# Kernel tuning notes

Hardware: AMD Instinct MI355X
Metric: run time of the kernel (lower is better)

## Reference

```python
import jax, jax.numpy as jnp
import numpy as np

N_HEAD = 16
D_HEAD = 64
D_MODEL = 1024
D_INNER = 4096
QLEN = 1024
MLEN = 1024
BSZ = 2
LN_EPS = 1e-5


def _layer_norm(x, g, b, eps=LN_EPS):
    mu = jnp.mean(x, axis=-1, keepdims=True)
    var = jnp.var(x, axis=-1, keepdims=True)
    return (x - mu) * jax.lax.rsqrt(var + eps) * g + b


def _rel_shift(x):
    # x: [qlen, rlen, bsz, n_head]
    q, r, b, n = x.shape
    zp = jnp.zeros((q, 1, b, n), x.dtype)
    xp = jnp.concatenate([zp, x], axis=1).reshape(r + 1, q, b, n)
    return xp[1:].reshape(q, r, b, n)


def setup_inputs() -> dict:
    key = jax.random.key(0)
    ks = jax.random.split(key, 12)
    klen = MLEN + QLEN
    w = jax.random.normal(ks[0], (QLEN, BSZ, D_MODEL), jnp.float32)
    r = jax.random.normal(ks[1], (klen, D_MODEL), jnp.float32)
    mems = jax.random.normal(ks[2], (MLEN, BSZ, D_MODEL), jnp.float32)
    # causal mask: query i attends keys j <= i + mlen
    i = jnp.arange(QLEN)[:, None]
    j = jnp.arange(klen)[None, :]
    attn_mask = (j > i + MLEN)[:, :, None]  # [qlen, klen, 1] bool
    s = 0.02
    params = dict(
        qkv_w=jax.random.normal(ks[3], (3 * N_HEAD * D_HEAD, D_MODEL), jnp.float32) * s,
        r_net_w=jax.random.normal(ks[4], (N_HEAD * D_HEAD, D_MODEL), jnp.float32) * s,
        o_w=jax.random.normal(ks[5], (D_MODEL, N_HEAD * D_HEAD), jnp.float32) * s,
        r_r_bias=jax.random.normal(ks[6], (N_HEAD, D_HEAD), jnp.float32) * s,
        r_w_bias=jax.random.normal(ks[7], (N_HEAD, D_HEAD), jnp.float32) * s,
        ln1_g=jnp.ones((D_MODEL,), jnp.float32),
        ln1_b=jnp.zeros((D_MODEL,), jnp.float32),
        ff_w1=jax.random.normal(ks[8], (D_INNER, D_MODEL), jnp.float32) * s,
        ff_b1=jnp.zeros((D_INNER,), jnp.float32),
        ff_w2=jax.random.normal(ks[9], (D_MODEL, D_INNER), jnp.float32) * s,
        ff_b2=jnp.zeros((D_MODEL,), jnp.float32),
        ln2_g=jnp.ones((D_MODEL,), jnp.float32),
        ln2_b=jnp.zeros((D_MODEL,), jnp.float32),
    )
    return dict(w=w, r=r, mems=mems, attn_mask=attn_mask, **params)


def reference(w, r, mems, attn_mask, qkv_w, r_net_w, o_w, r_r_bias, r_w_bias,
              ln1_g, ln1_b, ff_w1, ff_b1, ff_w2, ff_b2, ln2_g, ln2_b):
    qlen, bsz = w.shape[0], w.shape[1]
    scale = 1.0 / (D_HEAD ** 0.5)
    cat = jnp.concatenate([mems, w], axis=0)              # [klen, b, d_model]
    klen = cat.shape[0]
    w_heads = cat @ qkv_w.T                                # [klen, b, 3*n*d]
    wq, wk, wv = jnp.split(w_heads, 3, axis=-1)
    wq = wq[-qlen:]
    r_head_k = (r @ r_net_w.T).reshape(-1, N_HEAD, D_HEAD)  # [rlen, n, d]
    wq = wq.reshape(qlen, bsz, N_HEAD, D_HEAD)
    wk = wk.reshape(klen, bsz, N_HEAD, D_HEAD)
    wv = wv.reshape(klen, bsz, N_HEAD, D_HEAD)
    AC = jnp.einsum('ibnd,jbnd->ijbn', wq + r_w_bias, wk)   # content term
    BD = jnp.einsum('ibnd,jnd->ijbn', wq + r_r_bias, r_head_k)
    BD = _rel_shift(BD)                                     # position term
    attn_score = (AC + BD) * scale
    mask_value = jnp.finfo(attn_score.dtype).min
    attn_score = jnp.where(attn_mask[:, :, :, None], mask_value, attn_score)
    attn_prob = jax.nn.softmax(attn_score, axis=1)
    attn_vec = jnp.einsum('ijbn,jbnd->ibnd', attn_prob, wv)
    attn_vec = attn_vec.reshape(qlen, bsz, N_HEAD * D_HEAD)
    attn_out = attn_vec @ o_w.T
    h = _layer_norm(w + attn_out, ln1_g, ln1_b)             # post-lnorm
    core = jax.nn.relu(h @ ff_w1.T + ff_b1) @ ff_w2.T + ff_b2
    out = _layer_norm(h + core, ln2_g, ln2_b)
    return out
```

## Files before the change

### kernel.cpp

```cpp
#include <hip/hip_runtime.h>
#include <math.h>

#define QLEN 1024
#define MLEN 1024
#define KLEN 2048
#define BSZc 2
#define NH 16
#define DH 64
#define DM 1024
#define DI 4096

typedef unsigned short ushort_t;
typedef __attribute__((ext_vector_type(8))) short short8;
typedef __attribute__((ext_vector_type(4))) float f32x4;

__device__ __forceinline__ ushort_t f2bf(float x) {
    unsigned int u = __float_as_uint(x);
    unsigned int r = (u + 0x7FFFu + ((u >> 16) & 1u)) >> 16;
    return (ushort_t)r;
}
__device__ __forceinline__ float bf2f(ushort_t b) {
    return __uint_as_float(((unsigned int)b) << 16);
}

__device__ __forceinline__ void gload_lds16(const ushort_t* g, ushort_t* l) {
    __builtin_amdgcn_global_load_lds(
        (const __attribute__((address_space(1))) unsigned int*)g,
        (__attribute__((address_space(3))) unsigned int*)l,
        16, 0, 0);
}

__device__ __forceinline__ void cast8(const float* s, ushort_t* d, int g) {
    const float4 a = *(const float4*)(s + g * 8);
    const float4 b = *(const float4*)(s + g * 8 + 4);
    short8 o;
    o[0] = (short)f2bf(a.x); o[1] = (short)f2bf(a.y);
    o[2] = (short)f2bf(a.z); o[3] = (short)f2bf(a.w);
    o[4] = (short)f2bf(b.x); o[5] = (short)f2bf(b.y);
    o[6] = (short)f2bf(b.z); o[7] = (short)f2bf(b.w);
    *(short8*)(d + g * 8) = o;
}

__global__ __launch_bounds__(256)
void cast_phase1(const float* __restrict__ qkv_w, const float* __restrict__ rnet_w,
                 const float* __restrict__ mems, const float* __restrict__ w,
                 const float* __restrict__ r,
                 ushort_t* __restrict__ W1, ushort_t* __restrict__ W2,
                 ushort_t* __restrict__ Acat, ushort_t* __restrict__ Rsrc)
{
    int g = blockIdx.x * 256 + threadIdx.x;
    if (g < 393216)            { cast8(qkv_w,  W1,              g); }
    else if (g < 524288)       { cast8(rnet_w, W2,              g - 393216); }
    else if (g < 786432)       { cast8(mems,   Acat,            g - 524288); }
    else if (g < 1048576)      { cast8(w,      Acat + 2097152,  g - 786432); }
    else if (g < 1310720)      { cast8(r,      Rsrc,            g - 1048576); }
}

__global__ __launch_bounds__(256)
void cast_phase2(const float* __restrict__ o_w, const float* __restrict__ ffw1,
                 const float* __restrict__ ffw2,
                 ushort_t* __restrict__ W3, ushort_t* __restrict__ W4,
                 ushort_t* __restrict__ W5)
{
    int g = blockIdx.x * 256 + threadIdx.x;
    if (g < 131072)            { cast8(o_w,  W3, g); }
    else if (g < 655360)       { cast8(ffw1, W4, g - 131072); }
    else if (g < 1179648)      { cast8(ffw2, W5, g - 655360); }
}

template<int EMODE, int ACT, int BN>
__global__ __launch_bounds__(256)
void gemm_mfma(const ushort_t* __restrict__ A, const ushort_t* __restrict__ B,
               const float* __restrict__ bias,
               void* __restrict__ O0, void* __restrict__ O1,
               void* __restrict__ O2, void* __restrict__ O3,
               const float* __restrict__ rwb, const float* __restrict__ rrb,
               int M, int N, int K)
{
    constexpr int JT = BN / 32;
    __shared__ ushort_t At[128 * 32];
    __shared__ ushort_t Bt[BN * 32];

    const int tid  = threadIdx.x;
    const int lane = tid & 63;
    const int w    = tid >> 6;
    const int lr   = lane & 15;
    const int quad = lane >> 4;
    const int m0   = blockIdx.x * 128;
    const int n0   = blockIdx.y * BN;
    const int wm0  = (w >> 1) * 64;
    const int wn0  = (w & 1) * (BN / 2);

    f32x4 acc[4][JT];
#pragma unroll
    for (int it = 0; it < 4; ++it)
#pragma unroll
        for (int jt = 0; jt < JT; ++jt) acc[it][jt] = (f32x4){0.f, 0.f, 0.f, 0.f};

    const int srow = lane >> 2;
    const int scol = (lane & 3) << 3;
    const ushort_t* Ag = A + (size_t)(m0 + w * 32 + srow) * K + scol;
    ushort_t* lA0 = At + (w * 32) * 32;
    ushort_t* lA1 = At + (w * 32 + 16) * 32;
    const ushort_t* Bg;
    ushort_t *lB0, *lB1 = nullptr;
    if (BN == 128) {
        Bg  = B + (size_t)(n0 + w * 32 + srow) * K + scol;
        lB0 = Bt + (w * 32) * 32;
        lB1 = Bt + (w * 32 + 16) * 32;
    } else {
        Bg  = B + (size_t)(n0 + w * 16 + srow) * K + scol;
        lB0 = Bt + (w * 16) * 32;
    }

    const ushort_t* Ato = At + (wm0 + lr) * 32 + quad * 8;
    const ushort_t* Bto = Bt + (wn0 + lr) * 32 + quad * 8;

    for (int k0 = 0; k0 < K; k0 += 32) {
        __syncthreads();
        gload_lds16(Ag + k0, lA0);
        gload_lds16(Ag + (size_t)16 * K + k0, lA1);
        gload_lds16(Bg + k0, lB0);
        if (BN == 128) gload_lds16(Bg + (size_t)16 * K + k0, lB1);
        __syncthreads();

        short8 af[4], bf[JT];
#pragma unroll
        for (int it = 0; it < 4; ++it)
            af[it] = *(const short8*)(Ato + it * 16 * 32);
#pragma unroll
        for (int jt = 0; jt < JT; ++jt)
            bf[jt] = *(const short8*)(Bto + jt * 16 * 32);
#pragma unroll
        for (int it = 0; it < 4; ++it)
#pragma unroll
            for (int jt = 0; jt < JT; ++jt)
                acc[it][jt] = __builtin_amdgcn_mfma_f32_16x16x32_bf16(
                    af[it], bf[jt], acc[it][jt], 0, 0, 0);
    }

#pragma unroll
    for (int it = 0; it < 4; ++it)
#pragma unroll
        for (int jt = 0; jt < JT; ++jt)
#pragma unroll
            for (int rg = 0; rg < 4; ++rg) {
                const int m = m0 + wm0 + it * 16 + quad * 4 + rg;
                const int n = n0 + wn0 + jt * 16 + lr;
                float v = acc[it][jt][rg];
                if (EMODE == 0) {
                    if (bias) v += bias[n];
                    ((float*)O0)[(size_t)m * N + n] = v;
                } else if (EMODE == 1) {
                    const int j = m >> 1, b = m & 1;
                    const int part = n >> 10, hh = (n >> 6) & 15, d = n & 63;
                    if (part == 0) {
                        if (j >= MLEN) {
                            const int qi = j - MLEN;
                            const size_t qidx = (((size_t)(b * NH + hh)) * QLEN + qi) * DH + d;
                            ((ushort_t*)O0)[qidx] = f2bf(v + rwb[hh * DH + d]);
                            ((ushort_t*)O1)[qidx] = f2bf(v + rrb[hh * DH + d]);
                        }
                    } else if (part == 1) {
                        ((ushort_t*)O2)[(((size_t)(b * NH + hh)) * KLEN + j) * DH + d] = f2bf(v);
                    } else {
                        ((ushort_t*)O3)[(((size_t)(b * NH + hh)) * DH + d) * KLEN + j] = f2bf(v);
                    }
                } else if (EMODE == 2) {
                    const int hh = n >> 6, d = n & 63;
                    ((ushort_t*)O0)[(((size_t)hh) * KLEN + m) * DH + d] = f2bf(v);
                } else {
                    v += bias[n];
                    if (ACT == 1) v = fmaxf(v, 0.f);
                    ((ushort_t*)O0)[(size_t)m * N + n] = f2bf(v);
                }
            }
}

__global__ __launch_bounds__(256)
void attn_mfma(const ushort_t* __restrict__ Qac, const ushort_t* __restrict__ Qbd,
               const ushort_t* __restrict__ Kb, const ushort_t* __restrict__ Vt,
               const ushort_t* __restrict__ Rb, ushort_t* __restrict__ AV)
{
    __shared__ ushort_t Kt[64][72];
    __shared__ ushort_t Rt[128][72];
    __shared__ ushort_t Vl[64][72];
    __shared__ ushort_t Bw[4][16][84];

    const int tid  = threadIdx.x;
    const int lane = tid & 63;
    const int w    = tid >> 6;
    const int lr   = lane & 15;
    const int quad = lane >> 4;
    const int bh   = blockIdx.y;
    const int qt   = (bh & 16) ? (15 - (int)blockIdx.x) : (int)blockIdx.x;
    const int i0   = qt << 6;
    const int h    = bh & 15;
    const int b    = bh >> 4;

    short8 qaf[2], qbf[2];
    {
        const size_t rowoff = ((size_t)bh * QLEN + i0 + w * 16 + lr) * DH;
#pragma unroll
        for (int kt = 0; kt < 2; ++kt) {
            qaf[kt] = *(const short8*)(Qac + rowoff + kt * 32 + quad * 8);
            qbf[kt] = *(const short8*)(Qbd + rowoff + kt * 32 + quad * 8);
        }
    }

    f32x4 O[4];
#pragma unroll
    for (int nt = 0; nt < 4; ++nt) O[nt] = (f32x4){0.f, 0.f, 0.f, 0.f};
    float m_run = -3.4e38f, l_run = 0.f;

    const int nc  = qt + 17;
    const int stw = 3 - w;
    const float SC = 0.125f * 1.44269504f;
    const ushort_t* Kh = Kb + (size_t)bh * KLEN * DH;
    const ushort_t* Vh = Vt + (size_t)bh * DH * KLEN;
    const ushort_t* Rh = Rb + (size_t)h * KLEN * DH;

    for (int c = 0; c < nc; ++c) {
        const int j0 = c << 6;
        const int wb = 960 - i0 + j0;
        __syncthreads();
#pragma unroll
        for (int t = 0; t < 2; ++t) {
            int f = tid + (t << 8);
            int row = f >> 3, c8 = (f & 7) << 3;
            *(int4*)&Kt[row][c8] = *(const int4*)(Kh + (size_t)(j0 + row) * DH + c8);
        }
#pragma unroll
        for (int t = 0; t < 2; ++t) {
            int f = tid + (t << 8);
            int d = f >> 3, c8 = (f & 7) << 3;
            *(int4*)&Vl[d][c8] = *(const int4*)(Vh + (size_t)d * KLEN + j0 + c8);
        }
        {
            const int npass = (c == 0) ? 4 : 2;
            const int gb    = (c == 0) ? wb : wb + 64;
            for (int t = 0; t < npass; ++t) {
                int f = tid + (t << 8);
                int rl2 = f >> 3, c8 = (f & 7) << 3;
                int g = gb + rl2;
                int gc = g > (KLEN - 1) ? (KLEN - 1) : g;
                *(int4*)&Rt[g & 127][c8] = *(const int4*)(Rh + (size_t)gc * DH + c8);
            }
        }
        __syncthreads();

#pragma unroll
        for (int ctl = 0; ctl < 5; ++ctl) {
            const int wr = (stw + ctl) * 16 + lr;
            const int ring = (wb + wr) & 127;
            f32x4 z = (f32x4){0.f, 0.f, 0.f, 0.f};
#pragma unroll
            for (int kt = 0; kt < 2; ++kt) {
                short8 rb2 = *(const short8*)&Rt[ring][kt * 32 + quad * 8];
                z = __builtin_amdgcn_mfma_f32_16x16x32_bf16(qbf[kt], rb2, z, 0, 0, 0);
            }
#pragma unroll
            for (int rg = 0; rg < 4; ++rg)
                Bw[w][quad * 4 + rg][ctl * 16 + lr] = f2bf(z[rg]);
        }
#pragma unroll
        for (int ct = 0; ct < 4; ++ct) {
            f32x4 z = (f32x4){0.f, 0.f, 0.f, 0.f};
#pragma unroll
            for (int kt = 0; kt < 2; ++kt) {
                short8 kb2 = *(const short8*)&Kt[ct * 16 + lr][kt * 32 + quad * 8];
                z = __builtin_amdgcn_mfma_f32_16x16x32_bf16(qaf[kt], kb2, z, 0, 0, 0);
            }
#pragma unroll
            for (int rg = 0; rg < 4; ++rg) {
                const int rrow = quad * 4 + rg;
                ushort_t* p = &Bw[w][rrow][ct * 16 + lr + 15 - rrow];
                *p = f2bf(bf2f(*p) + z[rg]);
            }
        }

        const int lim = i0 + w * 16 + lr + 1024 - j0;
        float pv[16];
        float mx = -3.4e38f;
#pragma unroll
        for (int kt = 0; kt < 2; ++kt)
#pragma unroll
            for (int t = 0; t < 8; ++t) {
                const int jj = kt * 32 + quad * 8 + t;
                float s = bf2f(Bw[w][lr][jj + 15 - lr]) * SC;
                s = (jj > lim) ? -3.4e38f : s;
                pv[kt * 8 + t] = s;
                mx = fmaxf(mx, s);
            }
        mx = fmaxf(mx, __shfl_xor(mx, 16, 64));
        mx = fmaxf(mx, __shfl_xor(mx, 32, 64));
        const float m_new = fmaxf(m_run, mx);
        float ps = 0.f;
        short8 pf[2];
#pragma unroll
        for (int kt = 0; kt < 2; ++kt)
#pragma unroll
            for (int t = 0; t < 8; ++t) {
                const float e = exp2f(pv[kt * 8 + t] - m_new);
                ps += e;
                pf[kt][t] = (short)f2bf(e);
            }
        ps += __shfl_xor(ps, 16, 64);
        ps += __shfl_xor(ps, 32, 64);
        const float alpha = exp2f(m_run - m_new);
        m_run = m_new;
        l_run = l_run * alpha + ps;

        float ar[4];
#pragma unroll
        for (int rg = 0; rg < 4; ++rg)
            ar[rg] = __shfl(alpha, quad * 4 + rg, 64);
#pragma unroll
        for (int nt = 0; nt < 4; ++nt) {
            O[nt][0] *= ar[0]; O[nt][1] *= ar[1];
            O[nt][2] *= ar[2]; O[nt][3] *= ar[3];
        }
#pragma unroll
        for (int kt = 0; kt < 2; ++kt)
#pragma unroll
            for (int nt = 0; nt < 4; ++nt) {
                short8 vb = *(const short8*)&Vl[nt * 16 + lr][kt * 32 + quad * 8];
                O[nt] = __builtin_amdgcn_mfma_f32_16x16x32_bf16(pf[kt], vb, O[nt], 0, 0, 0);
            }
    }

    float rlv[4];
#pragma unroll
    for (int rg = 0; rg < 4; ++rg)
        rlv[rg] = 1.f / __shfl(l_run, quad * 4 + rg, 64);
#pragma unroll
    for (int nt = 0; nt < 4; ++nt)
#pragma unroll
        for (int rg = 0; rg < 4; ++rg) {
            const int i = i0 + w * 16 + quad * 4 + rg;
            AV[((size_t)i * BSZc + b) * DM + h * DH + nt * 16 + lr] = f2bf(O[nt][rg] * rlv[rg]);
        }
}

__global__ __launch_bounds__(256)
void add_ln(const float* __restrict__ X, const float* __restrict__ Y,
            const float* __restrict__ gg, const float* __restrict__ bb,
            float* __restrict__ out, ushort_t* __restrict__ outb)
{
    const int row  = blockIdx.x;
    const int tid  = threadIdx.x;
    const int lane = tid & 63;
    const int w    = tid >> 6;
    __shared__ float ssum[4], ssq[4];

    const float4 xv = ((const float4*)(X + (size_t)row * DM))[tid];
    const float4 yv = ((const float4*)(Y + (size_t)row * DM))[tid];
    const float v0 = xv.x + yv.x, v1 = xv.y + yv.y;
    const float v2 = xv.z + yv.z, v3 = xv.w + yv.w;
    float s = v0 + v1 + v2 + v3;
    float q = v0 * v0 + v1 * v1 + v2 * v2 + v3 * v3;
#pragma unroll
    for (int off = 32; off > 0; off >>= 1) {
        s += __shfl_xor(s, off, 64);
        q += __shfl_xor(q, off, 64);
    }
    if (lane == 0) { ssum[w] = s; ssq[w] = q; }
    __syncthreads();
    s = ssum[0] + ssum[1] + ssum[2] + ssum[3];
    q = ssq[0] + ssq[1] + ssq[2] + ssq[3];
    const float mean = s * (1.f / DM);
    const float var  = q * (1.f / DM) - mean * mean;
    const float rs   = rsqrtf(var + 1e-5f);
    const float4 g4 = ((const float4*)gg)[tid];
    const float4 b4 = ((const float4*)bb)[tid];
    float4 ov;
    ov.x = (v0 - mean) * rs * g4.x + b4.x;
    ov.y = (v1 - mean) * rs * g4.y + b4.y;
    ov.z = (v2 - mean) * rs * g4.z + b4.z;
    ov.w = (v3 - mean) * rs * g4.w + b4.w;
    ((float4*)(out + (size_t)row * DM))[tid] = ov;
    if (outb) {
        ushort_t* p = outb + (size_t)row * DM + tid * 4;
        p[0] = f2bf(ov.x); p[1] = f2bf(ov.y);
        p[2] = f2bf(ov.z); p[3] = f2bf(ov.w);
    }
}

extern "C" void kernel_launch(void* const* d_in, const int* in_sizes, int n_in,
                              void* d_out, int out_size, void* d_ws, size_t ws_size,
                              hipStream_t stream)
{
    (void)in_sizes; (void)n_in; (void)out_size; (void)ws_size;
    const float* w      = (const float*)d_in[0];
    const float* r      = (const float*)d_in[1];
    const float* mems   = (const float*)d_in[2];
    const float* qkv_w  = (const float*)d_in[4];
    const float* rnet_w = (const float*)d_in[5];
    const float* o_w    = (const float*)d_in[6];
    const float* r_r_b  = (const float*)d_in[7];
    const float* r_w_b  = (const float*)d_in[8];
    const float* ln1g   = (const float*)d_in[9];
    const float* ln1b   = (const float*)d_in[10];
    const float* ffw1   = (const float*)d_in[11];
    const float* ffb1   = (const float*)d_in[12];
    const float* ffw2   = (const float*)d_in[13];
    const float* ffb2   = (const float*)d_in[14];
    const float* ln2g   = (const float*)d_in[15];
    const float* ln2b   = (const float*)d_in[16];
    float* out = (float*)d_out;

    char* wsb = (char*)d_ws;
    const size_t MB = 1024 * 1024;
    ushort_t* W1    = (ushort_t*)(wsb + 0 * MB);
    ushort_t* W2    = (ushort_t*)(wsb + 6 * MB);
    ushort_t* Acat  = (ushort_t*)(wsb + 8 * MB);
    ushort_t* Rsrc  = (ushort_t*)(wsb + 16 * MB);
    ushort_t* Qac   = (ushort_t*)(wsb + 20 * MB);
    ushort_t* Qbd   = (ushort_t*)(wsb + 24 * MB);
    ushort_t* Kbf   = (ushort_t*)(wsb + 28 * MB);
    ushort_t* Vt    = (ushort_t*)(wsb + 36 * MB);
    ushort_t* Rh    = (ushort_t*)(wsb + 44 * MB);
    ushort_t* AVec  = (ushort_t*)(wsb + 0 * MB);
    ushort_t* W3    = (ushort_t*)(wsb + 4 * MB);
    float*    AOut  = (float*)(wsb + 8 * MB);
    float*    Hbuf  = (float*)(wsb + 16 * MB);
    ushort_t* Hbf   = (ushort_t*)(wsb + 24 * MB);
    ushort_t* W4    = (ushort_t*)(wsb + 28 * MB);
    ushort_t* FFbf  = (ushort_t*)(wsb + 36 * MB);
    ushort_t* W5    = (ushort_t*)(wsb + 52 * MB);
    float*    Core  = (float*)(wsb + 0 * MB);

    dim3 blk(256);

    cast_phase1<<<dim3(5120), blk, 0, stream>>>(qkv_w, rnet_w, mems, w, r,
                                                W1, W2, Acat, Rsrc);

    gemm_mfma<1, 0, 128><<<dim3(32, 24), blk, 0, stream>>>(
        Acat, W1, nullptr, Qac, Qbd, Kbf, Vt, r_w_b, r_r_b, 4096, 3072, 1024);

    gemm_mfma<2, 0, 64><<<dim3(16, 16), blk, 0, stream>>>(
        Rsrc, W2, nullptr, Rh, nullptr, nullptr, nullptr, nullptr, nullptr,
        2048, 1024, 1024);

    attn_mfma<<<dim3(QLEN / 64, BSZc * NH), blk, 0, stream>>>(
        Qac, Qbd, Kbf, Vt, Rh, AVec);

    cast_phase2<<<dim3(4608), blk, 0, stream>>>(o_w, ffw1, ffw2, W3, W4, W5);

    gemm_mfma<0, 0, 64><<<dim3(16, 16), blk, 0, stream>>>(
        AVec, W3, nullptr, AOut, nullptr, nullptr, nullptr, nullptr, nullptr,
        2048, 1024, 1024);

    add_ln<<<dim3(2 * QLEN), blk, 0, stream>>>(w, AOut, ln1g, ln1b, Hbuf, Hbf);

    gemm_mfma<3, 1, 128><<<dim3(16, 32), blk, 0, stream>>>(
        Hbf, W4, ffb1, FFbf, nullptr, nullptr, nullptr, nullptr, nullptr,
        2048, 4096, 1024);

    gemm_mfma<0, 0, 64><<<dim3(16, 16), blk, 0, stream>>>(
        FFbf, W5, ffb2, Core, nullptr, nullptr, nullptr, nullptr, nullptr,
        2048, 1024, 4096);

    add_ln<<<dim3(2 * QLEN), blk, 0, stream>>>(Hbuf, Core, ln2g, ln2b, out, nullptr);
}
```

Measured before the change: 460.0 us.

## Split attention KV range across two blocks, merge partials, fuse QKV and R GEMMs

The attention kernel now splits each query tile's key chunks between two blocks (even and odd chunks). Each block writes unnormalized fp32 partial outputs plus its running max and sum, and a new merge kernel combines them into the bf16 attention vector. This doubles the grid to raise occupancy on the many-CU GPU, at the cost of extra fp32 partial traffic and one more launch. The QKV and R projection GEMMs are fused into one launch. The position-score scratch moves from bf16 to fp32 and the R ring buffer is replaced by a full reload per chunk, which adds loads but removes the ring indexing.

```diff
diff --git a/kernel.cpp b/kernel.cpp
--- a/kernel.cpp
+++ b/kernel.cpp
@@ -18,9 +18,6 @@
     unsigned int u = __float_as_uint(x);
     unsigned int r = (u + 0x7FFFu + ((u >> 16) & 1u)) >> 16;
     return (ushort_t)r;
-}
-__device__ __forceinline__ float bf2f(ushort_t b) {
-    return __uint_as_float(((unsigned int)b) << 16);
 }
 
 __device__ __forceinline__ void gload_lds16(const ushort_t* g, ushort_t* l) {
@@ -72,10 +69,7 @@
 __global__ __launch_bounds__(256)
 void gemm_mfma(const ushort_t* __restrict__ A, const ushort_t* __restrict__ B,
                const float* __restrict__ bias,
-               void* __restrict__ O0, void* __restrict__ O1,
-               void* __restrict__ O2, void* __restrict__ O3,
-               const float* __restrict__ rwb, const float* __restrict__ rrb,
-               int M, int N, int K)
+               void* __restrict__ O0, int M, int N, int K)
 {
     constexpr int JT = BN / 32;
     __shared__ ushort_t At[128 * 32];
@@ -151,28 +145,108 @@
                 if (EMODE == 0) {
                     if (bias) v += bias[n];
                     ((float*)O0)[(size_t)m * N + n] = v;
-                } else if (EMODE == 1) {
+                } else {
+                    v += bias[n];
+                    if (ACT == 1) v = fmaxf(v, 0.f);
+                    ((ushort_t*)O0)[(size_t)m * N + n] = f2bf(v);
+                }
+            }
+}
+
+__global__ __launch_bounds__(256)
+void gemm_qkvr(const ushort_t* __restrict__ Acat, const ushort_t* __restrict__ W1,
+               const ushort_t* __restrict__ Rsrc, const ushort_t* __restrict__ W2,
+               ushort_t* __restrict__ Qac, ushort_t* __restrict__ Qbd,
+               ushort_t* __restrict__ Kbf, ushort_t* __restrict__ Vtb,
+               ushort_t* __restrict__ Rh,
+               const float* __restrict__ rwb, const float* __restrict__ rrb)
+{
+    __shared__ ushort_t At[128 * 32];
+    __shared__ ushort_t Bt[128 * 32];
+
+    const int bid  = blockIdx.x;
+    const bool isr = bid >= 768;
+    const ushort_t* A; const ushort_t* B; int m0, n0;
+    if (!isr) { A = Acat; B = W1; m0 = (bid & 31) * 128; n0 = (bid >> 5) * 128; }
+    else { int t = bid - 768; A = Rsrc; B = W2; m0 = (t & 15) * 128; n0 = (t >> 4) * 128; }
+    const int K = 1024;
+
+    const int tid  = threadIdx.x;
+    const int lane = tid & 63;
+    const int w    = tid >> 6;
+    const int lr   = lane & 15;
+    const int quad = lane >> 4;
+    const int wm0  = (w >> 1) * 64;
+    const int wn0  = (w & 1) * 64;
+
+    f32x4 acc[4][4];
+#pragma unroll
+    for (int it = 0; it < 4; ++it)
+#pragma unroll
+        for (int jt = 0; jt < 4; ++jt) acc[it][jt] = (f32x4){0.f, 0.f, 0.f, 0.f};
+
+    const int srow = lane >> 2;
+    const int scol = (lane & 3) << 3;
+    const ushort_t* Ag = A + (size_t)(m0 + w * 32 + srow) * K + scol;
+    const ushort_t* Bg = B + (size_t)(n0 + w * 32 + srow) * K + scol;
+    ushort_t* lA0 = At + (w * 32) * 32;
+    ushort_t* lA1 = At + (w * 32 + 16) * 32;
+    ushort_t* lB0 = Bt + (w * 32) * 32;
+    ushort_t* lB1 = Bt + (w * 32 + 16) * 32;
+
+    const ushort_t* Ato = At + (wm0 + lr) * 32 + quad * 8;
+    const ushort_t* Bto = Bt + (wn0 + lr) * 32 + quad * 8;
+
+    for (int k0 = 0; k0 < K; k0 += 32) {
+        __syncthreads();
+        gload_lds16(Ag + k0, lA0);
+        gload_lds16(Ag + (size_t)16 * K + k0, lA1);
+        gload_lds16(Bg + k0, lB0);
+        gload_lds16(Bg + (size_t)16 * K + k0, lB1);
+        __syncthreads();
+
+        short8 af[4], bf[4];
+#pragma unroll
+        for (int it = 0; it < 4; ++it)
+            af[it] = *(const short8*)(Ato + it * 16 * 32);
+#pragma unroll
+        for (int jt = 0; jt < 4; ++jt)
+            bf[jt] = *(const short8*)(Bto + jt * 16 * 32);
+#pragma unroll
+        for (int it = 0; it < 4; ++it)
+#pragma unroll
+            for (int jt = 0; jt < 4; ++jt)
+                acc[it][jt] = __builtin_amdgcn_mfma_f32_16x16x32_bf16(
+                    af[it], bf[jt], acc[it][jt], 0, 0, 0);
+    }
+
+#pragma unroll
+    for (int it = 0; it < 4; ++it)
+#pragma unroll
+        for (int jt = 0; jt < 4; ++jt)
+#pragma unroll
+            for (int rg = 0; rg < 4; ++rg) {
+                const int m = m0 + wm0 + it * 16 + quad * 4 + rg;
+                const int n = n0 + wn0 + jt * 16 + lr;
+                const float v = acc[it][jt][rg];
+                if (!isr) {
                     const int j = m >> 1, b = m & 1;
                     const int part = n >> 10, hh = (n >> 6) & 15, d = n & 63;
                     if (part == 0) {
                         if (j >= MLEN) {
                             const int qi = j - MLEN;
                             const size_t qidx = (((size_t)(b * NH + hh)) * QLEN + qi) * DH + d;
-                            ((ushort_t*)O0)[qidx] = f2bf(v + rwb[hh * DH + d]);
-                            ((ushort_t*)O1)[qidx] = f2bf(v + rrb[hh * DH + d]);
+                            Qac[qidx] = f2bf(v + rwb[hh * DH + d]);
+                            Qbd[qidx] = f2bf(v + rrb[hh * DH + d]);
                         }
                     } else if (part == 1) {
-                        ((ushort_t*)O2)[(((size_t)(b * NH + hh)) * KLEN + j) * DH + d] = f2bf(v);
+                        Kbf[(((size_t)(b * NH + hh)) * KLEN + j) * DH + d] = f2bf(v);
                     } else {
-                        ((ushort_t*)O3)[(((size_t)(b * NH + hh)) * DH + d) * KLEN + j] = f2bf(v);
+                        Vtb[(((size_t)(b * NH + hh)) * DH + d) * KLEN + j] = f2bf(v);
                     }
-                } else if (EMODE == 2) {
+                } else {
                     const int hh = n >> 6, d = n & 63;
-                    ((ushort_t*)O0)[(((size_t)hh) * KLEN + m) * DH + d] = f2bf(v);
-                } else {
-                    v += bias[n];
-                    if (ACT == 1) v = fmaxf(v, 0.f);
-                    ((ushort_t*)O0)[(size_t)m * N + n] = f2bf(v);
+                    Rh[(((size_t)hh) * KLEN + m) * DH + d] = f2bf(v);
                 }
             }
 }
@@ -180,20 +254,23 @@
 __global__ __launch_bounds__(256)
 void attn_mfma(const ushort_t* __restrict__ Qac, const ushort_t* __restrict__ Qbd,
                const ushort_t* __restrict__ Kb, const ushort_t* __restrict__ Vt,
-               const ushort_t* __restrict__ Rb, ushort_t* __restrict__ AV)
+               const ushort_t* __restrict__ Rb,
+               float* __restrict__ Op0, float* __restrict__ Op1,
+               float* __restrict__ Mp, float* __restrict__ Lp)
 {
     __shared__ ushort_t Kt[64][72];
     __shared__ ushort_t Rt[128][72];
     __shared__ ushort_t Vl[64][72];
-    __shared__ ushort_t Bw[4][16][84];
+    __shared__ float    Bw[4][16][84];
 
     const int tid  = threadIdx.x;
     const int lane = tid & 63;
     const int w    = tid >> 6;
     const int lr   = lane & 15;
     const int quad = lane >> 4;
-    const int bh   = blockIdx.y;
-    const int qt   = (bh & 16) ? (15 - (int)blockIdx.x) : (int)blockIdx.x;
+    const int qt   = blockIdx.x;
+    const int s    = blockIdx.y;
+    const int bh   = blockIdx.z;
     const int i0   = qt << 6;
     const int h    = bh & 15;
     const int b    = bh >> 4;
@@ -218,9 +295,9 @@
     const float SC = 0.125f * 1.44269504f;
     const ushort_t* Kh = Kb + (size_t)bh * KLEN * DH;
     const ushort_t* Vh = Vt + (size_t)bh * DH * KLEN;
-    const ushort_t* Rh = Rb + (size_t)h * KLEN * DH;
-
-    for (int c = 0; c < nc; ++c) {
+    const ushort_t* Rhp = Rb + (size_t)h * KLEN * DH;
+
+    for (int c = s; c < nc; c += 2) {
         const int j0 = c << 6;
         const int wb = 960 - i0 + j0;
         __syncthreads();
@@ -236,32 +313,28 @@
             int d = f >> 3, c8 = (f & 7) << 3;
             *(int4*)&Vl[d][c8] = *(const int4*)(Vh + (size_t)d * KLEN + j0 + c8);
         }
-        {
-            const int npass = (c == 0) ? 4 : 2;
-            const int gb    = (c == 0) ? wb : wb + 64;
-            for (int t = 0; t < npass; ++t) {
-                int f = tid + (t << 8);
-                int rl2 = f >> 3, c8 = (f & 7) << 3;
-                int g = gb + rl2;
-                int gc = g > (KLEN - 1) ? (KLEN - 1) : g;
-                *(int4*)&Rt[g & 127][c8] = *(const int4*)(Rh + (size_t)gc * DH + c8);
-            }
+#pragma unroll
+        for (int t = 0; t < 4; ++t) {
+            int f = tid + (t << 8);
+            int rl2 = f >> 3, c8 = (f & 7) << 3;
+            int g = wb + rl2;
+            int gc = g > (KLEN - 1) ? (KLEN - 1) : g;
+            *(int4*)&Rt[rl2][c8] = *(const int4*)(Rhp + (size_t)gc * DH + c8);
         }
         __syncthreads();
 
 #pragma unroll
         for (int ctl = 0; ctl < 5; ++ctl) {
             const int wr = (stw + ctl) * 16 + lr;
-            const int ring = (wb + wr) & 127;
             f32x4 z = (f32x4){0.f, 0.f, 0.f, 0.f};
 #pragma unroll
             for (int kt = 0; kt < 2; ++kt) {
-                short8 rb2 = *(const short8*)&Rt[ring][kt * 32 + quad * 8];
+                short8 rb2 = *(const short8*)&Rt[wr][kt * 32 + quad * 8];
                 z = __builtin_amdgcn_mfma_f32_16x16x32_bf16(qbf[kt], rb2, z, 0, 0, 0);
             }
 #pragma unroll
             for (int rg = 0; rg < 4; ++rg)
-                Bw[w][quad * 4 + rg][ctl * 16 + lr] = f2bf(z[rg]);
+                Bw[w][quad * 4 + rg][ctl * 16 + lr] = z[rg];
         }
 #pragma unroll
         for (int ct = 0; ct < 4; ++ct) {
@@ -274,8 +347,7 @@
 #pragma unroll
             for (int rg = 0; rg < 4; ++rg) {
                 const int rrow = quad * 4 + rg;
-                ushort_t* p = &Bw[w][rrow][ct * 16 + lr + 15 - rrow];
-                *p = f2bf(bf2f(*p) + z[rg]);
+                Bw[w][rrow][ct * 16 + lr + 15 - rrow] += z[rg];
             }
         }
 
@@ -287,10 +359,10 @@
 #pragma unroll
             for (int t = 0; t < 8; ++t) {
                 const int jj = kt * 32 + quad * 8 + t;
-                float s = bf2f(Bw[w][lr][jj + 15 - lr]) * SC;
-                s = (jj > lim) ? -3.4e38f : s;
-                pv[kt * 8 + t] = s;
-                mx = fmaxf(mx, s);
+                float sv = Bw[w][lr][jj + 15 - lr] * SC;
+                sv = (jj > lim) ? -3.4e38f : sv;
+                pv[kt * 8 + t] = sv;
+                mx = fmaxf(mx, sv);
             }
         mx = fmaxf(mx, __shfl_xor(mx, 16, 64));
         mx = fmaxf(mx, __shfl_xor(mx, 32, 64));
@@ -329,17 +401,45 @@
             }
     }
 
-    float rlv[4];
-#pragma unroll
-    for (int rg = 0; rg < 4; ++rg)
-        rlv[rg] = 1.f / __shfl(l_run, quad * 4 + rg, 64);
+    if (quad == 0) {
+        const size_t mi = ((size_t)s * 32 + bh) * QLEN + i0 + w * 16 + lr;
+        Mp[mi] = m_run;
+        Lp[mi] = l_run;
+    }
+    float* Op = s ? Op1 : Op0;
 #pragma unroll
     for (int nt = 0; nt < 4; ++nt)
 #pragma unroll
         for (int rg = 0; rg < 4; ++rg) {
             const int i = i0 + w * 16 + quad * 4 + rg;
-            AV[((size_t)i * BSZc + b) * DM + h * DH + nt * 16 + lr] = f2bf(O[nt][rg] * rlv[rg]);
-        }
+            Op[((size_t)i * BSZc + b) * DM + h * DH + nt * 16 + lr] = O[nt][rg];
+        }
+}
+
+__global__ __launch_bounds__(256)
+void attn_merge(const float* __restrict__ O0, const float* __restrict__ O1,
+                const float* __restrict__ Mp, const float* __restrict__ Lp,
+                ushort_t* __restrict__ AV)
+{
+    const int row = blockIdx.x;
+    const int tid = threadIdx.x;
+    const int i = row >> 1, b = row & 1;
+    const int h = tid >> 4;
+    const int bh = b * NH + h;
+    const size_t mi = (size_t)bh * QLEN + i;
+    const float m1 = Mp[mi],            l1 = Lp[mi];
+    const float m2 = Mp[32 * QLEN + mi], l2 = Lp[32 * QLEN + mi];
+    const float M = fmaxf(m1, m2);
+    const float a1 = exp2f(m1 - M), a2 = exp2f(m2 - M);
+    const float rl = 1.f / (l1 * a1 + l2 * a2);
+    const float f1 = a1 * rl, f2 = a2 * rl;
+    const float4 o1 = ((const float4*)(O0 + (size_t)row * DM))[tid];
+    const float4 o2 = ((const float4*)(O1 + (size_t)row * DM))[tid];
+    ushort_t* p = AV + (size_t)row * DM + tid * 4;
+    p[0] = f2bf(o1.x * f1 + o2.x * f2);
+    p[1] = f2bf(o1.y * f1 + o2.y * f2);
+    p[2] = f2bf(o1.z * f1 + o2.z * f2);
+    p[3] = f2bf(o1.w * f1 + o2.w * f2);
 }
 
 __global__ __launch_bounds__(256)
@@ -420,6 +520,10 @@
     ushort_t* Kbf   = (ushort_t*)(wsb + 28 * MB);
     ushort_t* Vt    = (ushort_t*)(wsb + 36 * MB);
     ushort_t* Rh    = (ushort_t*)(wsb + 44 * MB);
+    float*    Op0   = (float*)(wsb + 48 * MB);
+    float*    Op1   = (float*)(wsb + 56 * MB);
+    float*    Mp    = (float*)(wsb + 4 * MB);
+    float*    Lp    = (float*)(wsb + 4 * MB + 512 * 1024);
     ushort_t* AVec  = (ushort_t*)(wsb + 0 * MB);
     ushort_t* W3    = (ushort_t*)(wsb + 4 * MB);
     float*    AOut  = (float*)(wsb + 8 * MB);
@@ -435,31 +539,26 @@
     cast_phase1<<<dim3(5120), blk, 0, stream>>>(qkv_w, rnet_w, mems, w, r,
                                                 W1, W2, Acat, Rsrc);
 
-    gemm_mfma<1, 0, 128><<<dim3(32, 24), blk, 0, stream>>>(
-        Acat, W1, nullptr, Qac, Qbd, Kbf, Vt, r_w_b, r_r_b, 4096, 3072, 1024);
-
-    gemm_mfma<2, 0, 64><<<dim3(16, 16), blk, 0, stream>>>(
-        Rsrc, W2, nullptr, Rh, nullptr, nullptr, nullptr, nullptr, nullptr,
-        2048, 1024, 1024);
-
-    attn_mfma<<<dim3(QLEN / 64, BSZc * NH), blk, 0, stream>>>(
-        Qac, Qbd, Kbf, Vt, Rh, AVec);
+    gemm_qkvr<<<dim3(896), blk, 0, stream>>>(
+        Acat, W1, Rsrc, W2, Qac, Qbd, Kbf, Vt, Rh, r_w_b, r_r_b);
+
+    attn_mfma<<<dim3(16, 2, 32), blk, 0, stream>>>(
+        Qac, Qbd, Kbf, Vt, Rh, Op0, Op1, Mp, Lp);
+
+    attn_merge<<<dim3(2048), blk, 0, stream>>>(Op0, Op1, Mp, Lp, AVec);
 
     cast_phase2<<<dim3(4608), blk, 0, stream>>>(o_w, ffw1, ffw2, W3, W4, W5);
 
     gemm_mfma<0, 0, 64><<<dim3(16, 16), blk, 0, stream>>>(
-        AVec, W3, nullptr, AOut, nullptr, nullptr, nullptr, nullptr, nullptr,
-        2048, 1024, 1024);
+        AVec, W3, nullptr, AOut, 2048, 1024, 1024);
 
     add_ln<<<dim3(2 * QLEN), blk, 0, stream>>>(w, AOut, ln1g, ln1b, Hbuf, Hbf);
 
     gemm_mfma<3, 1, 128><<<dim3(16, 32), blk, 0, stream>>>(
-        Hbf, W4, ffb1, FFbf, nullptr, nullptr, nullptr, nullptr, nullptr,
-        2048, 4096, 1024);
+        Hbf, W4, ffb1, FFbf, 2048, 4096, 1024);
 
     gemm_mfma<0, 0, 64><<<dim3(16, 16), blk, 0, stream>>>(
-        FFbf, W5, ffb2, Core, nullptr, nullptr, nullptr, nullptr, nullptr,
-        2048, 1024, 4096);
+        FFbf, W5, ffb2, Core, 2048, 1024, 4096);
 
     add_ln<<<dim3(2 * QLEN), blk, 0, stream>>>(Hbuf, Core, ln2g, ln2b, out, nullptr);
 }
```

Result: faster. 440.6 us (-4.2%).
